# Kernel tuning notes

Measured on AMD Instinct MI355X. Metric: run time of the kernel, lower is better.

Reference implementation:

```python
import jax, jax.numpy as jnp
import numpy as np

B, NP, NL, CIN, COUT, MID = 2048, 8, 4, 256, 256, 64


def setup_inputs() -> dict:
    key = jax.random.key(0)
    ks = jax.random.split(key, 16)
    s = 0.01  # small init scale (code uses xavier_normal with tiny gain)
    inp = {
        "x": jax.random.normal(ks[0], (B, CIN), jnp.float32),
        "h": jax.random.normal(ks[1], (B, NP), jnp.float32),
        "index": jnp.zeros((NL,), jnp.float32).at[0].set(1.0),  # one-hot layer index
        # target Linear params
        "target_w": jax.random.normal(ks[2], (COUT, CIN), jnp.float32) * (1.0 / np.sqrt(CIN)),
        "target_b": jax.random.normal(ks[3], (COUT,), jnp.float32) * 0.01,
        # embedder weight branch
        "fcwp_w": jax.random.normal(ks[4], (MID * CIN, NP), jnp.float32) * s,
        "fcwp_b": jnp.zeros((MID * CIN,), jnp.float32),
        "fcwi_w": jax.random.normal(ks[5], (MID * CIN, NL), jnp.float32) * s,
        "fcwi_b": jnp.zeros((MID * CIN,), jnp.float32),
        "fcwe_w": jax.random.normal(ks[6], (COUT, MID), jnp.float32) * s,
        "fcwe_b": jnp.zeros((COUT,), jnp.float32),
        # embedder bias branch
        "fcbp_w": jax.random.normal(ks[7], (COUT, NP), jnp.float32) * s,
        "fcbp_b": jnp.zeros((COUT,), jnp.float32),
        "fcbi_w": jax.random.normal(ks[8], (COUT, NL), jnp.float32) * s,
        "fcbi_b": jnp.zeros((COUT,), jnp.float32),
    }
    return inp


def reference(x, h, index, target_w, target_b,
              fcwp_w, fcwp_b, fcwi_w, fcwi_b, fcwe_w, fcwe_b,
              fcbp_w, fcbp_b, fcbi_w, fcbi_b):
    # --- embedder: per-sample weight modulation ---
    # w_flat: (B, mid*cin)
    w_flat = h @ fcwp_w.T + fcwp_b + (index @ fcwi_w.T + fcwi_b)
    w = w_flat.reshape(B, CIN, MID)                      # (B, cin, mid)
    w = jnp.einsum('bim,om->boi', w, fcwe_w) + fcwe_b[None, :, None]  # swapaxes folded in -> (B, out, cin)
    # bias modulation: (B, out)
    b = h @ fcbp_w.T + fcbp_b + (index @ fcbi_w.T + fcbi_b)
    # --- per-sample linear (grouped conv2d == batched GEMM) ---
    weights = target_w[None] + w                         # (B, out, cin)
    y = jnp.einsum('bi,boi->bo', x, weights)             # batched matvec
    y = y + target_b[None, :] + b
    return y
```

## Files before the change

kernel.cpp:

```cpp
#include <hip/hip_runtime.h>


#define B_TOT 2048
#define NP    8
#define NL    4
#define CIN   256
#define COUT  256
#define MID   64
#define NBIG  896
#define LDSK  136

typedef short  short8  __attribute__((ext_vector_type(8)));
typedef float  floatx4 __attribute__((ext_vector_type(4)));

__device__ __forceinline__ unsigned short f2bf(float f) {
    union { float f; unsigned u; } v; v.f = f;
    unsigned r = v.u + 0x7FFFu + ((v.u >> 16) & 1u);
    return (unsigned short)(r >> 16);
}

__global__ __launch_bounds__(256) void setup_kernel(
    const float* __restrict__ x, const float* __restrict__ index,
    const float* __restrict__ target_w, const float* __restrict__ target_b,
    const float* __restrict__ fcwp_w, const float* __restrict__ fcwp_b,
    const float* __restrict__ fcwi_w, const float* __restrict__ fcwi_b,
    const float* __restrict__ fcbp_b,
    const float* __restrict__ fcbi_w, const float* __restrict__ fcbi_b,
    unsigned short* __restrict__ xbf, unsigned short* __restrict__ Bb,
    float* __restrict__ bias_const)
{
    int gid = blockIdx.x * 256 + threadIdx.x;
    if (gid < 131072) {
        float4 v = *(const float4*)(x + (size_t)gid * 4);
        ushort4 o;
        o.x = f2bf(v.x); o.y = f2bf(v.y); o.z = f2bf(v.z); o.w = f2bf(v.w);
        *(ushort4*)(xbf + (size_t)gid * 4) = o;
    } else if (gid < 262144) {
        int e = gid - 131072;
        int n = e & 511, i = e >> 9;
        Bb[n * CIN + i] = f2bf(fcwp_w[e]);
    } else if (gid < 278528) {
        int e = gid - 262144;
        int i = e >> 6, m = e & 63;
        float v = fcwp_b[e] + fcwi_b[e]
                + index[0] * fcwi_w[e * 4]     + index[1] * fcwi_w[e * 4 + 1]
                + index[2] * fcwi_w[e * 4 + 2] + index[3] * fcwi_w[e * 4 + 3];
        Bb[(512 + m) * CIN + i] = f2bf(v);
    } else if (gid < 344064) {
        int e = gid - 278528;
        Bb[576 * CIN + e] = f2bf(target_w[e]);
    } else if (gid < 344320) {
        Bb[832 * CIN + (gid - 344064)] = f2bf(1.0f);
    } else if (gid < 360448) {
        Bb[833 * CIN + (gid - 344320)] = 0;
    } else if (gid < 360704) {
        int o = gid - 360448;
        bias_const[o] = target_b[o] + fcbp_b[o] + fcbi_b[o]
                      + index[0] * fcbi_w[o * 4]     + index[1] * fcbi_w[o * 4 + 1]
                      + index[2] * fcbi_w[o * 4 + 2] + index[3] * fcbi_w[o * 4 + 3];
    }
}

__global__ __launch_bounds__(256) void gemm_kernel(
    const unsigned short* __restrict__ xbf,
    const unsigned short* __restrict__ Bb,
    float* __restrict__ Y)
{
    __shared__ unsigned short As[64][LDSK];
    __shared__ unsigned short Bs[64][LDSK];

    const int tid  = threadIdx.x;
    const int m_base = blockIdx.x * 64;
    const int n_base = blockIdx.y * 64;
    const int lane = tid & 63, w = tid >> 6;
    const int lrow = lane & 15, quad = lane >> 4;

    floatx4 acc[4] = {floatx4{0,0,0,0}, floatx4{0,0,0,0},
                      floatx4{0,0,0,0}, floatx4{0,0,0,0}};

    for (int kh = 0; kh < 2; ++kh) {
        const int k0 = kh * 128;
        __syncthreads();
        #pragma unroll
        for (int it = 0; it < 4; ++it) {
            int idx = tid + it * 256;
            int r = idx >> 4, cc = (idx & 15) * 8;
            uint4 av = *(const uint4*)(xbf + (size_t)(m_base + r) * CIN + k0 + cc);
            *(uint4*)&As[r][cc] = av;
            uint4 bv = *(const uint4*)(Bb  + (size_t)(n_base + r) * CIN + k0 + cc);
            *(uint4*)&Bs[r][cc] = bv;
        }
        __syncthreads();
        #pragma unroll
        for (int ks = 0; ks < 4; ++ks) {
            const int kc = ks * 32 + quad * 8;
            short8 af = *(const short8*)&As[w * 16 + lrow][kc];
            #pragma unroll
            for (int f = 0; f < 4; ++f) {
                short8 bfr = *(const short8*)&Bs[f * 16 + lrow][kc];
                acc[f] = __builtin_amdgcn_mfma_f32_16x16x32_bf16(af, bfr, acc[f], 0, 0, 0);
            }
        }
    }

    #pragma unroll
    for (int f = 0; f < 4; ++f)
        #pragma unroll
        for (int r = 0; r < 4; ++r)
            Y[(size_t)(m_base + w * 16 + quad * 4 + r) * NBIG + n_base + f * 16 + lrow]
                = acc[f][r];
}

__global__ __launch_bounds__(256) void epilogue_kernel(
    const float* __restrict__ Y,
    const float* __restrict__ h,
    const float* __restrict__ fcwe_w,
    const float* __restrict__ fcwe_b,
    const float* __restrict__ fcbp_w,
    const float* __restrict__ bias_const,
    float* __restrict__ out)
{
    __shared__ float tl[4][64];
    __shared__ float hl[4][NP];
    __shared__ float sxl[4];

    const int tid = threadIdx.x;
    const int b0  = blockIdx.x * 4;

    if (tid < 4 * NP) hl[tid >> 3][tid & 7] = h[(size_t)b0 * NP + tid];
    if (tid < 4)      sxl[tid] = Y[(size_t)(b0 + tid) * NBIG + 832];

    {
        int s = tid >> 6, m = tid & 63;
        const float* yr = Y + (size_t)(b0 + s) * NBIG;
        const float* hb = h + (size_t)(b0 + s) * NP;
        float4 u0 = *(const float4*)(yr + m * 8);
        float4 u1 = *(const float4*)(yr + m * 8 + 4);
        float t = yr[512 + m]
                + u0.x * hb[0] + u0.y * hb[1] + u0.z * hb[2] + u0.w * hb[3]
                + u1.x * hb[4] + u1.y * hb[5] + u1.z * hb[6] + u1.w * hb[7];
        tl[s][m] = t;
    }
    __syncthreads();

    const int o = tid;
    const float bc  = bias_const[o];
    const float web = fcwe_b[o];
    float y[4];
    #pragma unroll
    for (int s = 0; s < 4; ++s)
        y[s] = Y[(size_t)(b0 + s) * NBIG + 576 + o] + bc + web * sxl[s];

    const float* wer = fcwe_w + (size_t)o * MID;
    for (int mm = 0; mm < MID; mm += 4) {
        float4 w4 = *(const float4*)(wer + mm);
        #pragma unroll
        for (int s = 0; s < 4; ++s)
            y[s] += w4.x * tl[s][mm]     + w4.y * tl[s][mm + 1]
                  + w4.z * tl[s][mm + 2] + w4.w * tl[s][mm + 3];
    }
    const float* bpr = fcbp_w + (size_t)o * NP;
    float4 bp0 = *(const float4*)(bpr);
    float4 bp1 = *(const float4*)(bpr + 4);
    #pragma unroll
    for (int s = 0; s < 4; ++s)
        y[s] += bp0.x * hl[s][0] + bp0.y * hl[s][1] + bp0.z * hl[s][2] + bp0.w * hl[s][3]
              + bp1.x * hl[s][4] + bp1.y * hl[s][5] + bp1.z * hl[s][6] + bp1.w * hl[s][7];

    #pragma unroll
    for (int s = 0; s < 4; ++s)
        out[(size_t)(b0 + s) * COUT + o] = y[s];
}

extern "C" void kernel_launch(void* const* d_in, const int* in_sizes, int n_in,
                              void* d_out, int out_size, void* d_ws, size_t ws_size,
                              hipStream_t stream) {
    const float* x        = (const float*)d_in[0];
    const float* h        = (const float*)d_in[1];
    const float* index    = (const float*)d_in[2];
    const float* target_w = (const float*)d_in[3];
    const float* target_b = (const float*)d_in[4];
    const float* fcwp_w   = (const float*)d_in[5];
    const float* fcwp_b   = (const float*)d_in[6];
    const float* fcwi_w   = (const float*)d_in[7];
    const float* fcwi_b   = (const float*)d_in[8];
    const float* fcwe_w   = (const float*)d_in[9];
    const float* fcwe_b   = (const float*)d_in[10];
    const float* fcbp_w   = (const float*)d_in[11];
    const float* fcbp_b   = (const float*)d_in[12];
    const float* fcbi_w   = (const float*)d_in[13];
    const float* fcbi_b   = (const float*)d_in[14];
    float* out = (float*)d_out;

    char* ws = (char*)d_ws;
    float*          Y          = (float*)ws;
    unsigned short* xbf        = (unsigned short*)(ws + 7340032);
    unsigned short* Bb         = (unsigned short*)(ws + 8388608);
    float*          bias_const = (float*)(ws + 8847360);

    setup_kernel<<<1409, 256, 0, stream>>>(
        x, index, target_w, target_b, fcwp_w, fcwp_b, fcwi_w, fcwi_b,
        fcbp_b, fcbi_w, fcbi_b, xbf, Bb, bias_const);

    gemm_kernel<<<dim3(B_TOT / 64, NBIG / 64), 256, 0, stream>>>(xbf, Bb, Y);

    epilogue_kernel<<<B_TOT / 4, 256, 0, stream>>>(
        Y, h, fcwe_w, fcwe_b, fcbp_w, bias_const, out);
}
```

Measured before the change: 96.11 us.

## Fuse GEMM and epilogue into one kernel with MFMA second-stage contraction

The GEMM and epilogue kernels are merged into a single kernel. Each block handles 16 samples, converts x to bf16 in LDS, loops over 13 column tiles of the weight matrix, and reduces the h-weighted products on chip. The fcwe/fcbp/bias contraction becomes a second small MFMA GEMM against a packed B2 matrix. This drops the 7MB intermediate Y round trip and one launch. In exchange, only 128 blocks run, each working through a serial loop over tiles with many barriers, so occupancy is low.

```diff
diff --git a/kernel.cpp b/kernel.cpp
--- a/kernel.cpp
+++ b/kernel.cpp
@@ -3,12 +3,14 @@
 
 #define B_TOT 2048
 #define NP    8
-#define NL    4
 #define CIN   256
 #define COUT  256
 #define MID   64
-#define NBIG  896
-#define LDSK  136
+#define LDA   264
+#define LDB   264
+#define LDY   66
+#define LDT   72
+#define LDA2  104
 
 typedef short  short8  __attribute__((ext_vector_type(8)));
 typedef float  floatx4 __attribute__((ext_vector_type(4)));
@@ -18,158 +20,191 @@
     unsigned r = v.u + 0x7FFFu + ((v.u >> 16) & 1u);
     return (unsigned short)(r >> 16);
 }
+__device__ __forceinline__ float bf2f(unsigned short u) {
+    union { unsigned u; float f; } v; v.u = ((unsigned)u) << 16;
+    return v.f;
+}
 
 __global__ __launch_bounds__(256) void setup_kernel(
-    const float* __restrict__ x, const float* __restrict__ index,
+    const float* __restrict__ index,
     const float* __restrict__ target_w, const float* __restrict__ target_b,
     const float* __restrict__ fcwp_w, const float* __restrict__ fcwp_b,
     const float* __restrict__ fcwi_w, const float* __restrict__ fcwi_b,
-    const float* __restrict__ fcbp_b,
+    const float* __restrict__ fcwe_w, const float* __restrict__ fcwe_b,
+    const float* __restrict__ fcbp_w, const float* __restrict__ fcbp_b,
     const float* __restrict__ fcbi_w, const float* __restrict__ fcbi_b,
-    unsigned short* __restrict__ xbf, unsigned short* __restrict__ Bb,
-    float* __restrict__ bias_const)
+    unsigned short* __restrict__ Bb, unsigned short* __restrict__ B2)
 {
     int gid = blockIdx.x * 256 + threadIdx.x;
     if (gid < 131072) {
-        float4 v = *(const float4*)(x + (size_t)gid * 4);
-        ushort4 o;
-        o.x = f2bf(v.x); o.y = f2bf(v.y); o.z = f2bf(v.z); o.w = f2bf(v.w);
-        *(ushort4*)(xbf + (size_t)gid * 4) = o;
-    } else if (gid < 262144) {
-        int e = gid - 131072;
+        int e = gid;
         int n = e & 511, i = e >> 9;
         Bb[n * CIN + i] = f2bf(fcwp_w[e]);
-    } else if (gid < 278528) {
-        int e = gid - 262144;
+    } else if (gid < 147456) {
+        int e = gid - 131072;
         int i = e >> 6, m = e & 63;
         float v = fcwp_b[e] + fcwi_b[e]
                 + index[0] * fcwi_w[e * 4]     + index[1] * fcwi_w[e * 4 + 1]
                 + index[2] * fcwi_w[e * 4 + 2] + index[3] * fcwi_w[e * 4 + 3];
         Bb[(512 + m) * CIN + i] = f2bf(v);
-    } else if (gid < 344064) {
-        int e = gid - 278528;
+    } else if (gid < 212992) {
+        int e = gid - 147456;
         Bb[576 * CIN + e] = f2bf(target_w[e]);
-    } else if (gid < 344320) {
-        Bb[832 * CIN + (gid - 344064)] = f2bf(1.0f);
-    } else if (gid < 360448) {
-        Bb[833 * CIN + (gid - 344320)] = 0;
-    } else if (gid < 360704) {
-        int o = gid - 360448;
-        bias_const[o] = target_b[o] + fcbp_b[o] + fcbi_b[o]
-                      + index[0] * fcbi_w[o * 4]     + index[1] * fcbi_w[o * 4 + 1]
-                      + index[2] * fcbi_w[o * 4 + 2] + index[3] * fcbi_w[o * 4 + 3];
-    }
-}
-
-__global__ __launch_bounds__(256) void gemm_kernel(
-    const unsigned short* __restrict__ xbf,
+    } else if (gid < 229376) {
+        int e = gid - 212992;
+        int o = e >> 6, m = e & 63;
+        B2[o * 96 + m] = f2bf(fcwe_w[e]);
+    } else if (gid < 231424) {
+        int e = gid - 229376;
+        int o = e >> 3, p = e & 7;
+        B2[o * 96 + 64 + p] = f2bf(fcbp_w[e]);
+    } else if (gid < 231680) {
+        int o = gid - 231424;
+        B2[o * 96 + 72] = f2bf(fcwe_b[o]);
+        float bc = target_b[o] + fcbp_b[o] + fcbi_b[o]
+                 + index[0] * fcbi_w[o * 4]     + index[1] * fcbi_w[o * 4 + 1]
+                 + index[2] * fcbi_w[o * 4 + 2] + index[3] * fcbi_w[o * 4 + 3];
+        B2[o * 96 + 73] = f2bf(bc);
+        #pragma unroll
+        for (int z = 74; z < 96; ++z) B2[o * 96 + z] = 0;
+    }
+}
+
+__global__ __launch_bounds__(256) void fused_kernel(
+    const float* __restrict__ x,
+    const float* __restrict__ h,
     const unsigned short* __restrict__ Bb,
-    float* __restrict__ Y)
-{
-    __shared__ unsigned short As[64][LDSK];
-    __shared__ unsigned short Bs[64][LDSK];
-
-    const int tid  = threadIdx.x;
-    const int m_base = blockIdx.x * 64;
-    const int n_base = blockIdx.y * 64;
-    const int lane = tid & 63, w = tid >> 6;
-    const int lrow = lane & 15, quad = lane >> 4;
-
-    floatx4 acc[4] = {floatx4{0,0,0,0}, floatx4{0,0,0,0},
-                      floatx4{0,0,0,0}, floatx4{0,0,0,0}};
-
-    for (int kh = 0; kh < 2; ++kh) {
-        const int k0 = kh * 128;
-        __syncthreads();
-        #pragma unroll
-        for (int it = 0; it < 4; ++it) {
-            int idx = tid + it * 256;
-            int r = idx >> 4, cc = (idx & 15) * 8;
-            uint4 av = *(const uint4*)(xbf + (size_t)(m_base + r) * CIN + k0 + cc);
-            *(uint4*)&As[r][cc] = av;
-            uint4 bv = *(const uint4*)(Bb  + (size_t)(n_base + r) * CIN + k0 + cc);
-            *(uint4*)&Bs[r][cc] = bv;
-        }
-        __syncthreads();
-        #pragma unroll
-        for (int ks = 0; ks < 4; ++ks) {
-            const int kc = ks * 32 + quad * 8;
-            short8 af = *(const short8*)&As[w * 16 + lrow][kc];
-            #pragma unroll
-            for (int f = 0; f < 4; ++f) {
-                short8 bfr = *(const short8*)&Bs[f * 16 + lrow][kc];
-                acc[f] = __builtin_amdgcn_mfma_f32_16x16x32_bf16(af, bfr, acc[f], 0, 0, 0);
-            }
-        }
-    }
-
-    #pragma unroll
-    for (int f = 0; f < 4; ++f)
-        #pragma unroll
-        for (int r = 0; r < 4; ++r)
-            Y[(size_t)(m_base + w * 16 + quad * 4 + r) * NBIG + n_base + f * 16 + lrow]
-                = acc[f][r];
-}
-
-__global__ __launch_bounds__(256) void epilogue_kernel(
-    const float* __restrict__ Y,
-    const float* __restrict__ h,
-    const float* __restrict__ fcwe_w,
-    const float* __restrict__ fcwe_b,
-    const float* __restrict__ fcbp_w,
-    const float* __restrict__ bias_const,
+    const unsigned short* __restrict__ B2,
     float* __restrict__ out)
 {
-    __shared__ float tl[4][64];
-    __shared__ float hl[4][NP];
-    __shared__ float sxl[4];
-
-    const int tid = threadIdx.x;
-    const int b0  = blockIdx.x * 4;
-
-    if (tid < 4 * NP) hl[tid >> 3][tid & 7] = h[(size_t)b0 * NP + tid];
-    if (tid < 4)      sxl[tid] = Y[(size_t)(b0 + tid) * NBIG + 832];
+    __shared__ unsigned short As[16 * LDA];
+    __shared__ unsigned short Bs[64 * LDB];
+    __shared__ float Yt[16 * LDY];
+    __shared__ float tl[16][LDT];
+    __shared__ float hl[16][NP];
+    __shared__ float ps[16][16];
+    __shared__ float sxl[16];
+    __shared__ unsigned short A2[16 * LDA2];
+
+    const int tid  = threadIdx.x;
+    const int lane = tid & 63, w = tid >> 6;
+    const int col  = lane & 15, quad = lane >> 4;
+    const int b0   = blockIdx.x * 16;
+
+    #pragma unroll
+    for (int it = 0; it < 4; ++it) {
+        int idx = it * 256 + tid;
+        int r = idx >> 6, c = (idx & 63) * 4;
+        float4 v = *(const float4*)(x + (size_t)(b0 + r) * CIN + c);
+        ushort4 o4;
+        o4.x = f2bf(v.x); o4.y = f2bf(v.y); o4.z = f2bf(v.z); o4.w = f2bf(v.w);
+        *(ushort4*)&As[r * LDA + c] = o4;
+    }
+    if (tid < 16 * NP) hl[tid >> 3][tid & 7] = h[(size_t)b0 * NP + tid];
+    __syncthreads();
 
     {
-        int s = tid >> 6, m = tid & 63;
-        const float* yr = Y + (size_t)(b0 + s) * NBIG;
-        const float* hb = h + (size_t)(b0 + s) * NP;
-        float4 u0 = *(const float4*)(yr + m * 8);
-        float4 u1 = *(const float4*)(yr + m * 8 + 4);
-        float t = yr[512 + m]
-                + u0.x * hb[0] + u0.y * hb[1] + u0.z * hb[2] + u0.w * hb[3]
-                + u1.x * hb[4] + u1.y * hb[5] + u1.z * hb[6] + u1.w * hb[7];
-        tl[s][m] = t;
-    }
-    __syncthreads();
-
-    const int o = tid;
-    const float bc  = bias_const[o];
-    const float web = fcwe_b[o];
-    float y[4];
-    #pragma unroll
-    for (int s = 0; s < 4; ++s)
-        y[s] = Y[(size_t)(b0 + s) * NBIG + 576 + o] + bc + web * sxl[s];
-
-    const float* wer = fcwe_w + (size_t)o * MID;
-    for (int mm = 0; mm < MID; mm += 4) {
-        float4 w4 = *(const float4*)(wer + mm);
-        #pragma unroll
-        for (int s = 0; s < 4; ++s)
-            y[s] += w4.x * tl[s][mm]     + w4.y * tl[s][mm + 1]
-                  + w4.z * tl[s][mm + 2] + w4.w * tl[s][mm + 3];
-    }
-    const float* bpr = fcbp_w + (size_t)o * NP;
-    float4 bp0 = *(const float4*)(bpr);
-    float4 bp1 = *(const float4*)(bpr + 4);
-    #pragma unroll
-    for (int s = 0; s < 4; ++s)
-        y[s] += bp0.x * hl[s][0] + bp0.y * hl[s][1] + bp0.z * hl[s][2] + bp0.w * hl[s][3]
-              + bp1.x * hl[s][4] + bp1.y * hl[s][5] + bp1.z * hl[s][6] + bp1.w * hl[s][7];
-
-    #pragma unroll
-    for (int s = 0; s < 4; ++s)
-        out[(size_t)(b0 + s) * COUT + o] = y[s];
+        int s = tid >> 4, seg = tid & 15;
+        float p = 0.f;
+        #pragma unroll
+        for (int j = 0; j < 16; ++j) p += bf2f(As[s * LDA + seg * 16 + j]);
+        ps[s][seg] = p;
+    }
+    __syncthreads();
+    if (tid < 16) {
+        float p = 0.f;
+        #pragma unroll
+        for (int j = 0; j < 16; ++j) p += ps[tid][j];
+        sxl[tid] = p;
+    }
+
+    floatx4 ybase[4];
+
+    for (int nt = 0; nt < 13; ++nt) {
+        __syncthreads();
+        #pragma unroll
+        for (int it = 0; it < 8; ++it) {
+            int idx = it * 256 + tid;
+            int r = idx >> 5, ch = (idx & 31) * 8;
+            uint4 v = *(const uint4*)(Bb + (size_t)(nt * 64 + r) * CIN + ch);
+            *(uint4*)&Bs[r * LDB + ch] = v;
+        }
+        __syncthreads();
+
+        floatx4 acc = floatx4{0.f, 0.f, 0.f, 0.f};
+        #pragma unroll
+        for (int ks = 0; ks < 8; ++ks) {
+            int kc = ks * 32 + quad * 8;
+            short8 af = *(const short8*)&As[col * LDA + kc];
+            short8 bf = *(const short8*)&Bs[(w * 16 + col) * LDB + kc];
+            acc = __builtin_amdgcn_mfma_f32_16x16x32_bf16(af, bf, acc, 0, 0, 0);
+        }
+
+        if (nt < 8) {
+            #pragma unroll
+            for (int r = 0; r < 4; ++r)
+                Yt[(quad * 4 + r) * LDY + w * 16 + col] = acc[r];
+            __syncthreads();
+            if (tid < 128) {
+                int s = tid >> 3, ml = tid & 7;
+                float tv = 0.f;
+                #pragma unroll
+                for (int p = 0; p < NP; ++p)
+                    tv += hl[s][p] * Yt[s * LDY + ml * 8 + p];
+                tl[s][nt * 8 + ml] = tv;
+            }
+        } else if (nt == 8) {
+            #pragma unroll
+            for (int r = 0; r < 4; ++r)
+                Yt[(quad * 4 + r) * LDY + w * 16 + col] = acc[r];
+            __syncthreads();
+            #pragma unroll
+            for (int it = 0; it < 4; ++it) {
+                int idx = it * 256 + tid;
+                int s = idx >> 6, m = idx & 63;
+                tl[s][m] += Yt[s * LDY + m];
+            }
+        } else {
+            ybase[nt - 9] = acc;
+        }
+    }
+    __syncthreads();
+
+    #pragma unroll
+    for (int it = 0; it < 4; ++it) {
+        int idx = it * 256 + tid;
+        int s = idx >> 6, m = idx & 63;
+        A2[s * LDA2 + m] = f2bf(tl[s][m]);
+    }
+    if (tid < 128) A2[(tid >> 3) * LDA2 + 64 + (tid & 7)] = f2bf(hl[tid >> 3][tid & 7]);
+    if (tid < 16) {
+        A2[tid * LDA2 + 72] = f2bf(sxl[tid]);
+        A2[tid * LDA2 + 73] = 0x3F80;
+    }
+    for (int idx = tid; idx < 16 * 22; idx += 256) {
+        int s = idx / 22, cc = 74 + idx % 22;
+        A2[s * LDA2 + cc] = 0;
+    }
+    __syncthreads();
+
+    floatx4 y2[4];
+    #pragma unroll
+    for (int j = 0; j < 4; ++j) y2[j] = ybase[j];
+    #pragma unroll
+    for (int ks = 0; ks < 3; ++ks) {
+        int kc = ks * 32 + quad * 8;
+        short8 af = *(const short8*)&A2[col * LDA2 + kc];
+        #pragma unroll
+        for (int j = 0; j < 4; ++j) {
+            short8 bf = *(const short8*)(B2 + (size_t)(j * 64 + w * 16 + col) * 96 + kc);
+            y2[j] = __builtin_amdgcn_mfma_f32_16x16x32_bf16(af, bf, y2[j], 0, 0, 0);
+        }
+    }
+    #pragma unroll
+    for (int j = 0; j < 4; ++j)
+        #pragma unroll
+        for (int r = 0; r < 4; ++r)
+            out[(size_t)(b0 + quad * 4 + r) * COUT + j * 64 + w * 16 + col] = y2[j][r];
 }
 
 extern "C" void kernel_launch(void* const* d_in, const int* in_sizes, int n_in,
@@ -193,17 +228,12 @@
     float* out = (float*)d_out;
 
     char* ws = (char*)d_ws;
-    float*          Y          = (float*)ws;
-    unsigned short* xbf        = (unsigned short*)(ws + 7340032);
-    unsigned short* Bb         = (unsigned short*)(ws + 8388608);
-    float*          bias_const = (float*)(ws + 8847360);
-
-    setup_kernel<<<1409, 256, 0, stream>>>(
-        x, index, target_w, target_b, fcwp_w, fcwp_b, fcwi_w, fcwi_b,
-        fcbp_b, fcbi_w, fcbi_b, xbf, Bb, bias_const);
-
-    gemm_kernel<<<dim3(B_TOT / 64, NBIG / 64), 256, 0, stream>>>(xbf, Bb, Y);
-
-    epilogue_kernel<<<B_TOT / 4, 256, 0, stream>>>(
-        Y, h, fcwe_w, fcwe_b, fcbp_w, bias_const, out);
-}
+    unsigned short* Bb = (unsigned short*)ws;
+    unsigned short* B2 = (unsigned short*)(ws + 425984);
+
+    setup_kernel<<<905, 256, 0, stream>>>(
+        index, target_w, target_b, fcwp_w, fcwp_b, fcwi_w, fcwi_b,
+        fcwe_w, fcwe_b, fcbp_w, fcbp_b, fcbi_w, fcbi_b, Bb, B2);
+
+    fused_kernel<<<B_TOT / 16, 256, 0, stream>>>(x, h, Bb, B2, out);
+}
```

After: 99.90 us. 3.9% more time.
